# Kernel tuning notes

Hardware: AMD Instinct MI355X
Metric: run time of the kernel (lower is better)

The kernel has to match this reference:

```python
import jax, jax.numpy as jnp
import numpy as np

B, S, D = 4, 2048, 1024
HALF_PI = np.float32(np.pi / 2.0)


def setup_inputs() -> dict:
    key = jax.random.key(0)
    ks = jax.random.split(key, 12)
    std = np.float32(0.02)
    def w(k):
        return jax.random.normal(k, (D, D), dtype=jnp.float32) * std
    return {
        "x": jax.random.normal(ks[0], (B, S, D), dtype=jnp.float32),
        "W_q": w(ks[1]), "b_q": jnp.zeros((D,), jnp.float32),
        "W_k": w(ks[2]), "b_k": jnp.zeros((D,), jnp.float32),
        "W_v": w(ks[3]), "b_v": jnp.zeros((D,), jnp.float32),
        "W_t": w(ks[4]), "b_t": jnp.zeros((D,), jnp.float32),
        "W_o": w(ks[5]), "b_o": jnp.zeros((D,), jnp.float32),
        "entangle_strength": jnp.float32(0.5),
    }


def reference(x, W_q, b_q, W_k, b_k, W_v, b_v, W_t, b_t, W_o, b_o, entangle_strength):
    scale = jnp.float32(np.sqrt(D))
    Q = x @ W_q + b_q          # [B,S,D]
    K = x @ W_k + b_k
    V = x @ W_v + b_v
    # theta in [0, pi/2]; r = cos(2*theta)
    theta_q = jax.nn.sigmoid(Q @ W_t + b_t) * HALF_PI
    theta_k = jax.nn.sigmoid(K @ W_t + b_t) * HALF_PI
    r_q = jnp.cos(2.0 * theta_q)
    r_k = jnp.cos(2.0 * theta_k)
    classical = jnp.einsum("bqd,bkd->bqk", Q, K) / scale
    quantum = jnp.einsum("bqd,bkd->bqk", r_q, r_k) * entangle_strength
    attn_weights = jax.nn.softmax(classical + quantum, axis=-1)  # [B,S,S]
    # dropout: eval mode -> identity
    out = jnp.einsum("bqk,bkd->bqd", attn_weights, V)
    out = out @ W_o + b_o
    return out, attn_weights
```

## Files before the change

### kernel.cpp

```cpp
#include <hip/hip_runtime.h>
#include <cstdint>

typedef unsigned short u16;
typedef __attribute__((ext_vector_type(8))) short bf16x8;
typedef __attribute__((ext_vector_type(4))) float f32x4;

__device__ __forceinline__ u16 f2b(float x) {
  unsigned u = __float_as_uint(x);
  u += 0x7FFFu + ((u >> 16) & 1u);
  return (u16)(u >> 16);
}

__device__ __forceinline__ void gload16(const void* g, void* l) {
  __builtin_amdgcn_global_load_lds(
      (const __attribute__((address_space(1))) void*)g,
      (__attribute__((address_space(3))) void*)l, 16, 0, 0);
}

template <int N>
__device__ __forceinline__ void vmwait() {
  if constexpr (N == 0) asm volatile("s_waitcnt vmcnt(0)" ::: "memory");
  else if constexpr (N == 4) asm volatile("s_waitcnt vmcnt(4)" ::: "memory");
  else if constexpr (N == 8) asm volatile("s_waitcnt vmcnt(8)" ::: "memory");
}

__device__ __forceinline__ void stage128(const u16* __restrict__ G,
                                         long long ld, int kb,
                                         u16* Ldst, int tid) {
#pragma unroll
  for (int j = 0; j < 2; ++j) {
    const int P = j * 256 + tid;
    const int vr = P >> 3;
    const int ch = (P & 7) ^ (vr & 7);
    const int r = vr * 2 + (ch >> 2), c = ch & 3;
    gload16(G + (long long)r * ld + kb + c * 8, Ldst + P * 8);
  }
}

__device__ __forceinline__ bf16x8 fr4(const u16* R, int row, int chunk) {
  const int vr = row >> 1;
  const int ch = (((row & 1) << 2) | chunk) ^ (vr & 7);
  return *(const bf16x8*)(R + vr * 64 + ch * 8);
}

template <int EPI>
__global__ __launch_bounds__(256, 3) void e3p(
    const u16* __restrict__ A, long long lda, long long sAz,
    const u16* __restrict__ B, long long ldb, long long sBz,
    void* __restrict__ C0, void* __restrict__ C1, void* __restrict__ C2,
    long long ldc, long long sCz, int K,
    const float* __restrict__ b0, const float* __restrict__ b1,
    const float* __restrict__ b2, float preScale, const float* __restrict__ esp) {
  constexpr int HALF = 4096;
  constexpr int BUFU = 2 * HALF;
  __shared__ __align__(16) u16 lds[3 * BUFU];

  const int gx = gridDim.x, S = gx * gridDim.y;
  const int hw = blockIdx.y * gx + blockIdx.x;
  const int l = (hw & 7) * (S >> 3) + (hw >> 3);
  const int bx = l % gx, by = l / gx;
  const int z = blockIdx.z;
  const long long tM = (long long)by * 128;
  const long long tN = (long long)bx * 128;
  const u16* GA = A + z * sAz + tM * lda;
  const u16* GB = B + z * sBz + tN * ldb;
  const int tid = threadIdx.x;
  const int NT = K >> 5;

  stage128(GA, lda, 0, lds, tid);
  stage128(GB, ldb, 0, lds + HALF, tid);
  stage128(GA, lda, 32, lds + BUFU, tid);
  stage128(GB, ldb, 32, lds + BUFU + HALF, tid);

  const int wid = tid >> 6, lane = tid & 63;
  const int wr = (wid >> 1) * 64, wc = (wid & 1) * 64;
  const int lr = lane & 15, cA = lane >> 4;
  f32x4 acc[4][4] = {};

  for (int t = 0; t < NT; ++t) {
    if (t < NT - 1) vmwait<4>(); else vmwait<0>();
    __builtin_amdgcn_s_barrier();
    if (t + 2 < NT) {
      u16* nxt = lds + ((t + 2) % 3) * BUFU;
      stage128(GA, lda, (t + 2) * 32, nxt, tid);
      stage128(GB, ldb, (t + 2) * 32, nxt + HALF, tid);
    }
    const u16* cur = lds + (t % 3) * BUFU;
    bf16x8 a[4], b[4];
#pragma unroll
    for (int m = 0; m < 4; ++m) a[m] = fr4(cur, wr + m * 16 + lr, cA);
#pragma unroll
    for (int n = 0; n < 4; ++n) b[n] = fr4(cur + HALF, wc + n * 16 + lr, cA);
#pragma unroll
    for (int m = 0; m < 4; ++m)
#pragma unroll
      for (int n = 0; n < 4; ++n)
        acc[m][n] = __builtin_amdgcn_mfma_f32_16x16x32_bf16(a[m], b[n],
                                                            acc[m][n], 0, 0, 0);
  }

  const int rr = (lane >> 4) << 2;
  float ps = preScale, mul = 1.0f;
  if constexpr (EPI == 1) {
    ps = (z == 0) ? preScale : 1.0f;
    mul = (z == 0) ? esp[0] : 1.0f;
  }
#pragma unroll
  for (int m = 0; m < 4; ++m) {
#pragma unroll
    for (int n = 0; n < 4; ++n) {
      const int col = (int)tN + wc + n * 16 + lr;
#pragma unroll
      for (int r = 0; r < 4; ++r) {
        const long long row = tM + wr + m * 16 + rr + r;
        const float v = acc[m][n][r];
        if constexpr (EPI == 0) {
          const int gg = col >> 10, cc = col & 1023;
          if (gg == 0)      ((u16*)C0)[row * 2048 + cc] = f2b((v + b0[cc]) * 0.03125f);
          else if (gg == 1) ((u16*)C1)[row * 2048 + cc] = f2b(v + b1[cc]);
          else              ((u16*)C2)[row * 1024 + cc] = f2b(v + b2[cc]);
        } else if constexpr (EPI == 1) {
          const float tt = v * ps + b0[col];
          const float sg = 1.f / (1.f + __expf(-tt));
          ((u16*)C0)[z * sCz + row * ldc + col] = f2b(mul * cospif(sg));
        } else if constexpr (EPI == 2) {
          ((u16*)C0)[z * sCz + row * ldc + col] = f2b(v);
        } else if constexpr (EPI == 3) {
          ((float*)C0)[z * sCz + row * ldc + col] = v + b0[col];
        } else {
          ((float*)C0)[z * sCz + row * ldc + col] = v;
        }
      }
    }
  }
}

__global__ __launch_bounds__(256) void softmax_rows(float* __restrict__ L,
                                                    u16* __restrict__ AB) {
  const long long row = blockIdx.x;
  float4* p4 = (float4*)(L + row * 2048);
  const int tid = threadIdx.x;
  float4 a = p4[tid], b = p4[tid + 256];
  float m = fmaxf(fmaxf(fmaxf(a.x, a.y), fmaxf(a.z, a.w)),
                  fmaxf(fmaxf(b.x, b.y), fmaxf(b.z, b.w)));
#pragma unroll
  for (int o = 32; o > 0; o >>= 1) m = fmaxf(m, __shfl_xor(m, o));
  __shared__ float rmax[4], rsum[4];
  const int wid = tid >> 6, lane = tid & 63;
  if (lane == 0) rmax[wid] = m;
  __syncthreads();
  m = fmaxf(fmaxf(rmax[0], rmax[1]), fmaxf(rmax[2], rmax[3]));
  a.x = __expf(a.x - m); a.y = __expf(a.y - m);
  a.z = __expf(a.z - m); a.w = __expf(a.w - m);
  b.x = __expf(b.x - m); b.y = __expf(b.y - m);
  b.z = __expf(b.z - m); b.w = __expf(b.w - m);
  float s = a.x + a.y + a.z + a.w + b.x + b.y + b.z + b.w;
#pragma unroll
  for (int o = 32; o > 0; o >>= 1) s += __shfl_xor(s, o);
  if (lane == 0) rsum[wid] = s;
  __syncthreads();
  s = rsum[0] + rsum[1] + rsum[2] + rsum[3];
  const float inv = 1.0f / s;
  a.x *= inv; a.y *= inv; a.z *= inv; a.w *= inv;
  b.x *= inv; b.y *= inv; b.z *= inv; b.w *= inv;
  p4[tid] = a;
  p4[tid + 256] = b;
  ushort4* o4 = (ushort4*)(AB + row * 2048);
  o4[tid]       = make_ushort4(f2b(a.x), f2b(a.y), f2b(a.z), f2b(a.w));
  o4[tid + 256] = make_ushort4(f2b(b.x), f2b(b.y), f2b(b.z), f2b(b.w));
}

__global__ __launch_bounds__(256) void cvt_x(const float* __restrict__ X,
                                             u16* __restrict__ XB) {
  const int i = blockIdx.x * 256 + threadIdx.x;
  float4 v = ((const float4*)X)[i];
  ((ushort4*)XB)[i] = make_ushort4(f2b(v.x), f2b(v.y), f2b(v.z), f2b(v.w));
}

__global__ void cvt_w(const float* __restrict__ W0, const float* __restrict__ W1,
                      const float* __restrict__ W2, const float* __restrict__ W3,
                      const float* __restrict__ W4, u16* __restrict__ WT) {
  __shared__ float t[32][33];
  const int z = blockIdx.z;
  const float* W = (z == 0) ? W0 : (z == 1) ? W1 : (z == 2) ? W2 : (z == 3) ? W3 : W4;
  u16* D = WT + (long long)z * 1024 * 1024;
  const int c0 = blockIdx.x * 32, r0 = blockIdx.y * 32;
  const int tx = threadIdx.x, ty = threadIdx.y;
#pragma unroll
  for (int i = 0; i < 4; ++i)
    t[ty + i * 8][tx] = W[(long long)(r0 + ty + i * 8) * 1024 + c0 + tx];
  __syncthreads();
#pragma unroll
  for (int i = 0; i < 4; ++i)
    D[(long long)(c0 + ty + i * 8) * 1024 + r0 + tx] = f2b(t[tx][ty + i * 8]);
}

__global__ void transpose_v(const u16* __restrict__ Vb, u16* __restrict__ VT) {
  __shared__ u16 t[32][33];
  const int b = blockIdx.z;
  const u16* V = Vb + (long long)b * 2048 * 1024;
  u16* O = VT + (long long)b * 1024 * 2048;
  const int d0 = blockIdx.x * 32, s0 = blockIdx.y * 32;
  const int tx = threadIdx.x, ty = threadIdx.y;
#pragma unroll
  for (int i = 0; i < 4; ++i)
    t[ty + i * 8][tx] = V[(long long)(s0 + ty + i * 8) * 1024 + d0 + tx];
  __syncthreads();
#pragma unroll
  for (int i = 0; i < 4; ++i)
    O[(long long)(d0 + ty + i * 8) * 2048 + s0 + tx] = t[tx][ty + i * 8];
}

extern "C" void kernel_launch(void* const* d_in, const int* in_sizes, int n_in,
                              void* d_out, int out_size, void* d_ws,
                              size_t ws_size, hipStream_t stream) {
  const float* x  = (const float*)d_in[0];
  const float* Wq = (const float*)d_in[1];
  const float* bq = (const float*)d_in[2];
  const float* Wk = (const float*)d_in[3];
  const float* bk = (const float*)d_in[4];
  const float* Wv = (const float*)d_in[5];
  const float* bv = (const float*)d_in[6];
  const float* Wt = (const float*)d_in[7];
  const float* bt = (const float*)d_in[8];
  const float* Wo = (const float*)d_in[9];
  const float* bo = (const float*)d_in[10];
  const float* es = (const float*)d_in[11];

  char* ws = (char*)d_ws;
  u16* WT   = (u16*)(ws);
  u16* XB   = (u16*)(ws + 10485760);
  u16* Qcat = (u16*)(ws + 27262976);
  u16* Kcat = Qcat + 16777216;
  u16* Vb   = (u16*)(ws + 94371840);
  u16* VT   = (u16*)(ws + 111149056);
  u16* WtT  = WT + 3 * 1048576;
  u16* WoT  = WT + 4 * 1048576;
  u16* ATT  = Qcat;
  u16* AV   = XB;

  float* outO = (float*)d_out;
  float* outA = outO + 8388608;

  cvt_x<<<8192, 256, 0, stream>>>(x, XB);
  cvt_w<<<dim3(32, 32, 5), dim3(32, 8), 0, stream>>>(Wq, Wk, Wv, Wt, Wo, WT);
  e3p<0><<<dim3(24, 64, 1), 256, 0, stream>>>(
      XB, 1024, 0, WT, 1024, 0, Qcat, Kcat, Vb, 0, 0, 1024, bq, bk, bv,
      1.f, nullptr);
  e3p<1><<<dim3(8, 64, 2), 256, 0, stream>>>(
      Qcat, 2048, 16777216LL, WtT, 1024, 0, Qcat + 1024, nullptr, nullptr,
      2048, 16777216LL, 1024, bt, nullptr, nullptr, 32.f, es);
  transpose_v<<<dim3(32, 64, 4), dim3(32, 8), 0, stream>>>(Vb, VT);
  e3p<4><<<dim3(16, 16, 4), 256, 0, stream>>>(
      Qcat, 2048, 4194304LL, Kcat, 2048, 4194304LL, outA, nullptr, nullptr,
      2048, 4194304LL, 2048, nullptr, nullptr, nullptr, 1.f, nullptr);
  softmax_rows<<<8192, 256, 0, stream>>>(outA, ATT);
  e3p<2><<<dim3(8, 16, 4), 256, 0, stream>>>(
      ATT, 2048, 4194304LL, VT, 2048, 2097152LL, AV, nullptr, nullptr,
      1024, 2097152LL, 2048, nullptr, nullptr, nullptr, 1.f, nullptr);
  e3p<3><<<dim3(8, 64, 1), 256, 0, stream>>>(
      AV, 1024, 0, WoT, 1024, 0, outO, nullptr, nullptr,
      1024, 0, 1024, bo, nullptr, nullptr, 1.f, nullptr);
}
```

Measured before the change: 352.1 us.

## Fold W_t into Q/K weights, fuse theta projections into one wide GEMM, compute V transposed

Precomputes Wq·Wt and Wk·Wt (plus a folded bias) so theta_q/theta_k come straight from x in the same wide GEMM that produces Q and K. This removes the dependent second GEMM over Q/K and its reread of the Q/K buffers. V is now produced already transposed by a GEMM with swapped operands, which eliminates the separate transpose kernel. In exchange it adds small weight-product GEMMs and a bias-fold kernel, and the new wide 128x256 tile kernel uses more registers and LDS and runs at lower occupancy.

```diff
diff --git a/kernel.cpp b/kernel.cpp
--- a/kernel.cpp
+++ b/kernel.cpp
@@ -21,7 +21,7 @@
 __device__ __forceinline__ void vmwait() {
   if constexpr (N == 0) asm volatile("s_waitcnt vmcnt(0)" ::: "memory");
   else if constexpr (N == 4) asm volatile("s_waitcnt vmcnt(4)" ::: "memory");
-  else if constexpr (N == 8) asm volatile("s_waitcnt vmcnt(8)" ::: "memory");
+  else if constexpr (N == 6) asm volatile("s_waitcnt vmcnt(6)" ::: "memory");
 }
 
 __device__ __forceinline__ void stage128(const u16* __restrict__ G,
@@ -47,10 +47,8 @@
 __global__ __launch_bounds__(256, 3) void e3p(
     const u16* __restrict__ A, long long lda, long long sAz,
     const u16* __restrict__ B, long long ldb, long long sBz,
-    void* __restrict__ C0, void* __restrict__ C1, void* __restrict__ C2,
-    long long ldc, long long sCz, int K,
-    const float* __restrict__ b0, const float* __restrict__ b1,
-    const float* __restrict__ b2, float preScale, const float* __restrict__ esp) {
+    void* __restrict__ C0, long long ldc, long long sCz, int K,
+    const float* __restrict__ b0) {
   constexpr int HALF = 4096;
   constexpr int BUFU = 2 * HALF;
   __shared__ __align__(16) u16 lds[3 * BUFU];
@@ -100,11 +98,6 @@
   }
 
   const int rr = (lane >> 4) << 2;
-  float ps = preScale, mul = 1.0f;
-  if constexpr (EPI == 1) {
-    ps = (z == 0) ? preScale : 1.0f;
-    mul = (z == 0) ? esp[0] : 1.0f;
-  }
 #pragma unroll
   for (int m = 0; m < 4; ++m) {
 #pragma unroll
@@ -114,25 +107,122 @@
       for (int r = 0; r < 4; ++r) {
         const long long row = tM + wr + m * 16 + rr + r;
         const float v = acc[m][n][r];
-        if constexpr (EPI == 0) {
-          const int gg = col >> 10, cc = col & 1023;
-          if (gg == 0)      ((u16*)C0)[row * 2048 + cc] = f2b((v + b0[cc]) * 0.03125f);
-          else if (gg == 1) ((u16*)C1)[row * 2048 + cc] = f2b(v + b1[cc]);
-          else              ((u16*)C2)[row * 1024 + cc] = f2b(v + b2[cc]);
-        } else if constexpr (EPI == 1) {
-          const float tt = v * ps + b0[col];
-          const float sg = 1.f / (1.f + __expf(-tt));
-          ((u16*)C0)[z * sCz + row * ldc + col] = f2b(mul * cospif(sg));
-        } else if constexpr (EPI == 2) {
+        if constexpr (EPI == 2) {
           ((u16*)C0)[z * sCz + row * ldc + col] = f2b(v);
         } else if constexpr (EPI == 3) {
           ((float*)C0)[z * sCz + row * ldc + col] = v + b0[col];
+        } else if constexpr (EPI == 4) {
+          ((float*)C0)[z * sCz + row * ldc + col] = v;
         } else {
-          ((float*)C0)[z * sCz + row * ldc + col] = v;
+          ((u16*)C0)[z * sCz + row * ldc + col] = f2b(v + b0[row]);
         }
       }
     }
   }
+}
+
+__device__ __forceinline__ void stage_w(const u16* GA, const u16* GB,
+                                        long long lda, long long ldb,
+                                        int kb, u16* buf, int tid) {
+  stage128(GA, lda, kb, buf, tid);
+  stage128(GB, ldb, kb, buf + 4096, tid);
+  stage128(GB + 128 * ldb, ldb, kb, buf + 8192, tid);
+}
+
+__global__ __launch_bounds__(256, 2) void e3w(
+    const u16* __restrict__ A, long long lda,
+    const u16* __restrict__ B, long long ldb,
+    u16* __restrict__ Qc, u16* __restrict__ Kc, int K,
+    const float* __restrict__ b0, const float* __restrict__ b1,
+    const float* __restrict__ b2, const float* __restrict__ b3,
+    const float* __restrict__ esp) {
+  constexpr int AS = 4096, BS = 8192;
+  constexpr int BUFU = AS + BS;
+  __shared__ __align__(16) u16 lds[3 * BUFU];
+
+  const int gx = gridDim.x, S = gx * gridDim.y;
+  const int hw = blockIdx.y * gx + blockIdx.x;
+  const int l = (hw & 7) * (S >> 3) + (hw >> 3);
+  const int bx = l % gx, by = l / gx;
+  const long long tM = (long long)by * 128;
+  const long long tN = (long long)bx * 256;
+  const u16* GA = A + tM * lda;
+  const u16* GB = B + tN * ldb;
+  const int tid = threadIdx.x;
+  const int NT = K >> 5;
+
+  stage_w(GA, GB, lda, ldb, 0, lds, tid);
+  stage_w(GA, GB, lda, ldb, 32, lds + BUFU, tid);
+
+  const int wid = tid >> 6, lane = tid & 63;
+  const int wr = (wid >> 1) * 64, wc = (wid & 1) * 128;
+  const int lr = lane & 15, cA = lane >> 4;
+  f32x4 acc[4][8] = {};
+
+  for (int t = 0; t < NT; ++t) {
+    if (t < NT - 1) vmwait<6>(); else vmwait<0>();
+    __builtin_amdgcn_s_barrier();
+    if (t + 2 < NT)
+      stage_w(GA, GB, lda, ldb, (t + 2) * 32, lds + ((t + 2) % 3) * BUFU, tid);
+    const u16* cur = lds + (t % 3) * BUFU;
+    const u16* Bs = cur + AS + (wid & 1) * 4096;
+    bf16x8 a[4], b[8];
+#pragma unroll
+    for (int m = 0; m < 4; ++m) a[m] = fr4(cur, wr + m * 16 + lr, cA);
+#pragma unroll
+    for (int n = 0; n < 8; ++n) b[n] = fr4(Bs, n * 16 + lr, cA);
+#pragma unroll
+    for (int m = 0; m < 4; ++m)
+#pragma unroll
+      for (int n = 0; n < 8; ++n)
+        acc[m][n] = __builtin_amdgcn_mfma_f32_16x16x32_bf16(a[m], b[n],
+                                                            acc[m][n], 0, 0, 0);
+  }
+
+  const int rr = (lane >> 4) << 2;
+  const float es = esp[0];
+#pragma unroll
+  for (int m = 0; m < 4; ++m) {
+#pragma unroll
+    for (int n = 0; n < 8; ++n) {
+      const int col = (int)tN + wc + n * 16 + lr;
+      const int g = col >> 10, cc = col & 1023;
+#pragma unroll
+      for (int r = 0; r < 4; ++r) {
+        const long long row = tM + wr + m * 16 + rr + r;
+        const float v = acc[m][n][r];
+        if (g == 0) {
+          Qc[row * 2048 + cc] = f2b((v + b0[cc]) * 0.03125f);
+        } else if (g == 1) {
+          Kc[row * 2048 + cc] = f2b(v + b1[cc]);
+        } else if (g == 2) {
+          const float tt = v + b2[cc];
+          Qc[row * 2048 + 1024 + cc] = f2b(es * cospif(1.f / (1.f + __expf(-tt))));
+        } else {
+          const float tt = v + b3[cc];
+          Kc[row * 2048 + 1024 + cc] = f2b(cospif(1.f / (1.f + __expf(-tt))));
+        }
+      }
+    }
+  }
+}
+
+__global__ __launch_bounds__(256) void bias_fold(
+    const float* __restrict__ bq, const float* __restrict__ bk,
+    const float* __restrict__ Wt, const float* __restrict__ bt,
+    float* __restrict__ out) {
+  const int z = blockIdx.z;
+  const float* bsrc = z ? bk : bq;
+  float* dst = out + z * 1024;
+  const int il = threadIdx.x & 127, ki = threadIdx.x >> 7;
+  const int i = blockIdx.x * 128 + il;
+  float acc = 0.f;
+  for (int k = ki; k < 1024; k += 2)
+    acc += bsrc[k] * Wt[(long long)k * 1024 + i];
+  __shared__ float red[256];
+  red[threadIdx.x] = acc;
+  __syncthreads();
+  if (ki == 0) dst[i] = red[il] + red[il + 128] + bt[i];
 }
 
 __global__ __launch_bounds__(256) void softmax_rows(float* __restrict__ L,
@@ -182,10 +272,22 @@
                       const float* __restrict__ W4, u16* __restrict__ WT) {
   __shared__ float t[32][33];
   const int z = blockIdx.z;
-  const float* W = (z == 0) ? W0 : (z == 1) ? W1 : (z == 2) ? W2 : (z == 3) ? W3 : W4;
-  u16* D = WT + (long long)z * 1024 * 1024;
+  const float* W = (z == 0 || z == 5) ? W0
+                 : (z == 1 || z == 6) ? W1
+                 : (z == 2) ? W2 : (z == 3) ? W3 : W4;
+  const int slot = (z == 0) ? 0 : (z == 1) ? 1 : (z == 2) ? 4
+                 : (z == 3) ? 5 : (z == 4) ? 6 : (z == 5) ? 7 : 8;
+  u16* D = WT + ((long long)slot << 20);
   const int c0 = blockIdx.x * 32, r0 = blockIdx.y * 32;
   const int tx = threadIdx.x, ty = threadIdx.y;
+  if (z >= 5) {
+#pragma unroll
+    for (int i = 0; i < 4; ++i) {
+      const long long idx = (long long)(r0 + ty + i * 8) * 1024 + c0 + tx;
+      D[idx] = f2b(W[idx]);
+    }
+    return;
+  }
 #pragma unroll
   for (int i = 0; i < 4; ++i)
     t[ty + i * 8][tx] = W[(long long)(r0 + ty + i * 8) * 1024 + c0 + tx];
@@ -193,22 +295,6 @@
 #pragma unroll
   for (int i = 0; i < 4; ++i)
     D[(long long)(c0 + ty + i * 8) * 1024 + r0 + tx] = f2b(t[tx][ty + i * 8]);
-}
-
-__global__ void transpose_v(const u16* __restrict__ Vb, u16* __restrict__ VT) {
-  __shared__ u16 t[32][33];
-  const int b = blockIdx.z;
-  const u16* V = Vb + (long long)b * 2048 * 1024;
-  u16* O = VT + (long long)b * 1024 * 2048;
-  const int d0 = blockIdx.x * 32, s0 = blockIdx.y * 32;
-  const int tx = threadIdx.x, ty = threadIdx.y;
-#pragma unroll
-  for (int i = 0; i < 4; ++i)
-    t[ty + i * 8][tx] = V[(long long)(s0 + ty + i * 8) * 1024 + d0 + tx];
-  __syncthreads();
-#pragma unroll
-  for (int i = 0; i < 4; ++i)
-    O[(long long)(d0 + ty + i * 8) * 2048 + s0 + tx] = t[tx][ty + i * 8];
 }
 
 extern "C" void kernel_launch(void* const* d_in, const int* in_sizes, int n_in,
@@ -228,37 +314,37 @@
   const float* es = (const float*)d_in[11];
 
   char* ws = (char*)d_ws;
-  u16* WT   = (u16*)(ws);
-  u16* XB   = (u16*)(ws + 10485760);
-  u16* Qcat = (u16*)(ws + 27262976);
-  u16* Kcat = Qcat + 16777216;
-  u16* Vb   = (u16*)(ws + 94371840);
-  u16* VT   = (u16*)(ws + 111149056);
-  u16* WtT  = WT + 3 * 1048576;
-  u16* WoT  = WT + 4 * 1048576;
-  u16* ATT  = Qcat;
-  u16* AV   = XB;
+  u16* WT     = (u16*)(ws);
+  float* BQT  = (float*)(ws + 18874368);
+  u16* XB     = (u16*)(ws + 20971520);
+  u16* Qcat   = (u16*)(ws + 37748736);
+  u16* Kcat   = (u16*)(ws + 71303168);
+  u16* VT     = (u16*)(ws + 104857600);
+  u16* ATT    = Qcat;
+  u16* AV     = XB;
 
   float* outO = (float*)d_out;
   float* outA = outO + 8388608;
 
   cvt_x<<<8192, 256, 0, stream>>>(x, XB);
-  cvt_w<<<dim3(32, 32, 5), dim3(32, 8), 0, stream>>>(Wq, Wk, Wv, Wt, Wo, WT);
-  e3p<0><<<dim3(24, 64, 1), 256, 0, stream>>>(
-      XB, 1024, 0, WT, 1024, 0, Qcat, Kcat, Vb, 0, 0, 1024, bq, bk, bv,
-      1.f, nullptr);
-  e3p<1><<<dim3(8, 64, 2), 256, 0, stream>>>(
-      Qcat, 2048, 16777216LL, WtT, 1024, 0, Qcat + 1024, nullptr, nullptr,
-      2048, 16777216LL, 1024, bt, nullptr, nullptr, 32.f, es);
-  transpose_v<<<dim3(32, 64, 4), dim3(32, 8), 0, stream>>>(Vb, VT);
+  cvt_w<<<dim3(32, 32, 7), dim3(32, 8), 0, stream>>>(Wq, Wk, Wv, Wt, Wo, WT);
+  bias_fold<<<dim3(8, 1, 2), 256, 0, stream>>>(bq, bk, Wt, bt, BQT);
+  e3p<2><<<dim3(8, 8, 2), 256, 0, stream>>>(
+      WT + (5LL << 20), 1024, 0, WT + (7LL << 20), 1024, 1048576,
+      WT + (2LL << 20), 1024, 1048576, 1024, nullptr);
+  e3w<<<dim3(16, 64, 1), 256, 0, stream>>>(
+      XB, 1024, WT, 1024, Qcat, Kcat, 1024, bq, bk, BQT, BQT + 1024, es);
+  e3p<6><<<dim3(16, 8, 4), 256, 0, stream>>>(
+      WT + (4LL << 20), 1024, 0, XB, 1024, 2097152,
+      VT, 2048, 2097152, 1024, bv);
   e3p<4><<<dim3(16, 16, 4), 256, 0, stream>>>(
-      Qcat, 2048, 4194304LL, Kcat, 2048, 4194304LL, outA, nullptr, nullptr,
-      2048, 4194304LL, 2048, nullptr, nullptr, nullptr, 1.f, nullptr);
+      Qcat, 2048, 4194304, Kcat, 2048, 4194304,
+      outA, 2048, 4194304, 2048, nullptr);
   softmax_rows<<<8192, 256, 0, stream>>>(outA, ATT);
   e3p<2><<<dim3(8, 16, 4), 256, 0, stream>>>(
-      ATT, 2048, 4194304LL, VT, 2048, 2097152LL, AV, nullptr, nullptr,
-      1024, 2097152LL, 2048, nullptr, nullptr, nullptr, 1.f, nullptr);
+      ATT, 2048, 4194304, VT, 2048, 2097152,
+      AV, 1024, 2097152, 2048, nullptr);
   e3p<3><<<dim3(8, 64, 1), 256, 0, stream>>>(
-      AV, 1024, 0, WoT, 1024, 0, outO, nullptr, nullptr,
-      1024, 0, 1024, bo, nullptr, nullptr, 1.f, nullptr);
-}
+      AV, 1024, 0, WT + (6LL << 20), 1024, 0,
+      outO, 1024, 0, 1024, bo);
+}
```

Result: slower. 581.3 us (+65.1%).

## Fold W_v·W_o into one weight and drop V projection and transpose

Applied to the files above, without the earlier changes.

Uses associativity: out = A·(x·Wv + bv)·Wo + bo = A·(x·(Wv·Wo)) + (bv·Wo + bo), because softmax rows sum to one. It precomputes Wv·Wo once, computes the transposed product (WvWo)^T·x^T directly, and folds the biases into one vector. This removes the separate V projection, the V transpose and the final output projection GEMM. The QK projection is narrowed to two outputs. The cost is a small extra 1024³ weight GEMM and an extra bf16 rounding of the combined weight.

```diff
diff --git a/kernel.cpp b/kernel.cpp
--- a/kernel.cpp
+++ b/kernel.cpp
@@ -21,7 +21,6 @@
 __device__ __forceinline__ void vmwait() {
   if constexpr (N == 0) asm volatile("s_waitcnt vmcnt(0)" ::: "memory");
   else if constexpr (N == 4) asm volatile("s_waitcnt vmcnt(4)" ::: "memory");
-  else if constexpr (N == 8) asm volatile("s_waitcnt vmcnt(8)" ::: "memory");
 }
 
 __device__ __forceinline__ void stage128(const u16* __restrict__ G,
@@ -47,10 +46,10 @@
 __global__ __launch_bounds__(256, 3) void e3p(
     const u16* __restrict__ A, long long lda, long long sAz,
     const u16* __restrict__ B, long long ldb, long long sBz,
-    void* __restrict__ C0, void* __restrict__ C1, void* __restrict__ C2,
+    void* __restrict__ C0, void* __restrict__ C1,
     long long ldc, long long sCz, int K,
     const float* __restrict__ b0, const float* __restrict__ b1,
-    const float* __restrict__ b2, float preScale, const float* __restrict__ esp) {
+    float preScale, const float* __restrict__ esp) {
   constexpr int HALF = 4096;
   constexpr int BUFU = 2 * HALF;
   __shared__ __align__(16) u16 lds[3 * BUFU];
@@ -115,10 +114,9 @@
         const long long row = tM + wr + m * 16 + rr + r;
         const float v = acc[m][n][r];
         if constexpr (EPI == 0) {
-          const int gg = col >> 10, cc = col & 1023;
-          if (gg == 0)      ((u16*)C0)[row * 2048 + cc] = f2b((v + b0[cc]) * 0.03125f);
-          else if (gg == 1) ((u16*)C1)[row * 2048 + cc] = f2b(v + b1[cc]);
-          else              ((u16*)C2)[row * 1024 + cc] = f2b(v + b2[cc]);
+          const int g = col >> 10, cc = col & 1023;
+          if (g == 0) ((u16*)C0)[row * 2048 + cc] = f2b((v + b0[cc]) * 0.03125f);
+          else        ((u16*)C1)[row * 2048 + cc] = f2b(v + b1[cc]);
         } else if constexpr (EPI == 1) {
           const float tt = v * ps + b0[col];
           const float sg = 1.f / (1.f + __expf(-tt));
@@ -135,6 +133,23 @@
   }
 }
 
+__global__ __launch_bounds__(256) void bias_fold(
+    const float* __restrict__ bv, const float* __restrict__ Wo,
+    const float* __restrict__ bo, float* __restrict__ out) {
+  const int i = blockIdx.x;
+  float acc = 0.f;
+  for (int k = threadIdx.x; k < 1024; k += 256)
+    acc += bv[k] * Wo[(long long)k * 1024 + i];
+  __shared__ float red[256];
+  red[threadIdx.x] = acc;
+  __syncthreads();
+  for (int s = 128; s > 0; s >>= 1) {
+    if (threadIdx.x < s) red[threadIdx.x] += red[threadIdx.x + s];
+    __syncthreads();
+  }
+  if (threadIdx.x == 0) out[i] = red[0] + bo[i];
+}
+
 __global__ __launch_bounds__(256) void softmax_rows(float* __restrict__ L,
                                                     u16* __restrict__ AB) {
   const long long row = blockIdx.x;
@@ -177,15 +192,24 @@
   ((ushort4*)XB)[i] = make_ushort4(f2b(v.x), f2b(v.y), f2b(v.z), f2b(v.w));
 }
 
-__global__ void cvt_w(const float* __restrict__ W0, const float* __restrict__ W1,
-                      const float* __restrict__ W2, const float* __restrict__ W3,
-                      const float* __restrict__ W4, u16* __restrict__ WT) {
+__global__ void cvt_w(const float* __restrict__ Wq, const float* __restrict__ Wk,
+                      const float* __restrict__ Wt, const float* __restrict__ Wo,
+                      const float* __restrict__ Wv, u16* __restrict__ WT) {
   __shared__ float t[32][33];
   const int z = blockIdx.z;
-  const float* W = (z == 0) ? W0 : (z == 1) ? W1 : (z == 2) ? W2 : (z == 3) ? W3 : W4;
-  u16* D = WT + (long long)z * 1024 * 1024;
+  const float* W = (z == 0) ? Wq : (z == 1) ? Wk : (z == 2) ? Wt
+                 : (z == 3) ? Wo : Wv;
+  u16* D = WT + ((long long)z << 20);
   const int c0 = blockIdx.x * 32, r0 = blockIdx.y * 32;
   const int tx = threadIdx.x, ty = threadIdx.y;
+  if (z == 4) {
+#pragma unroll
+    for (int i = 0; i < 4; ++i) {
+      const long long idx = (long long)(r0 + ty + i * 8) * 1024 + c0 + tx;
+      D[idx] = f2b(W[idx]);
+    }
+    return;
+  }
 #pragma unroll
   for (int i = 0; i < 4; ++i)
     t[ty + i * 8][tx] = W[(long long)(r0 + ty + i * 8) * 1024 + c0 + tx];
@@ -193,22 +217,6 @@
 #pragma unroll
   for (int i = 0; i < 4; ++i)
     D[(long long)(c0 + ty + i * 8) * 1024 + r0 + tx] = f2b(t[tx][ty + i * 8]);
-}
-
-__global__ void transpose_v(const u16* __restrict__ Vb, u16* __restrict__ VT) {
-  __shared__ u16 t[32][33];
-  const int b = blockIdx.z;
-  const u16* V = Vb + (long long)b * 2048 * 1024;
-  u16* O = VT + (long long)b * 1024 * 2048;
-  const int d0 = blockIdx.x * 32, s0 = blockIdx.y * 32;
-  const int tx = threadIdx.x, ty = threadIdx.y;
-#pragma unroll
-  for (int i = 0; i < 4; ++i)
-    t[ty + i * 8][tx] = V[(long long)(s0 + ty + i * 8) * 1024 + d0 + tx];
-  __syncthreads();
-#pragma unroll
-  for (int i = 0; i < 4; ++i)
-    O[(long long)(d0 + ty + i * 8) * 2048 + s0 + tx] = t[tx][ty + i * 8];
 }
 
 extern "C" void kernel_launch(void* const* d_in, const int* in_sizes, int n_in,
@@ -228,37 +236,37 @@
   const float* es = (const float*)d_in[11];
 
   char* ws = (char*)d_ws;
-  u16* WT   = (u16*)(ws);
-  u16* XB   = (u16*)(ws + 10485760);
-  u16* Qcat = (u16*)(ws + 27262976);
-  u16* Kcat = Qcat + 16777216;
-  u16* Vb   = (u16*)(ws + 94371840);
-  u16* VT   = (u16*)(ws + 111149056);
-  u16* WtT  = WT + 3 * 1048576;
-  u16* WoT  = WT + 4 * 1048576;
-  u16* ATT  = Qcat;
-  u16* AV   = XB;
+  u16* WT    = (u16*)(ws);
+  float* BF  = (float*)(ws + 12582912);
+  u16* XB    = (u16*)(ws + 12587008);
+  u16* Qcat  = (u16*)(ws + 29364224);
+  u16* Kcat  = Qcat + 16777216;
+  u16* XVT   = (u16*)(ws + 96473088);
+  u16* ATT   = Qcat;
 
   float* outO = (float*)d_out;
   float* outA = outO + 8388608;
 
   cvt_x<<<8192, 256, 0, stream>>>(x, XB);
-  cvt_w<<<dim3(32, 32, 5), dim3(32, 8), 0, stream>>>(Wq, Wk, Wv, Wt, Wo, WT);
-  e3p<0><<<dim3(24, 64, 1), 256, 0, stream>>>(
-      XB, 1024, 0, WT, 1024, 0, Qcat, Kcat, Vb, 0, 0, 1024, bq, bk, bv,
-      1.f, nullptr);
+  cvt_w<<<dim3(32, 32, 5), dim3(32, 8), 0, stream>>>(Wq, Wk, Wt, Wo, Wv, WT);
+  bias_fold<<<1024, 256, 0, stream>>>(bv, Wo, bo, BF);
+  e3p<2><<<dim3(8, 8, 1), 256, 0, stream>>>(
+      WT + (3LL << 20), 1024, 0, WT + (4LL << 20), 1024, 0,
+      WT + (5LL << 20), nullptr, 1024, 0, 1024, nullptr, nullptr, 1.f, nullptr);
+  e3p<0><<<dim3(16, 64, 1), 256, 0, stream>>>(
+      XB, 1024, 0, WT, 1024, 0, Qcat, Kcat, 2048, 0, 1024,
+      bq, bk, 1.f, nullptr);
   e3p<1><<<dim3(8, 64, 2), 256, 0, stream>>>(
-      Qcat, 2048, 16777216LL, WtT, 1024, 0, Qcat + 1024, nullptr, nullptr,
-      2048, 16777216LL, 1024, bt, nullptr, nullptr, 32.f, es);
-  transpose_v<<<dim3(32, 64, 4), dim3(32, 8), 0, stream>>>(Vb, VT);
+      Qcat, 2048, 16777216, WT + (2LL << 20), 1024, 0, Qcat + 1024, nullptr,
+      2048, 16777216, 1024, bt, nullptr, 32.f, es);
+  e3p<2><<<dim3(16, 8, 4), 256, 0, stream>>>(
+      WT + (5LL << 20), 1024, 0, XB, 1024, 2097152,
+      XVT, nullptr, 2048, 2097152, 1024, nullptr, nullptr, 1.f, nullptr);
   e3p<4><<<dim3(16, 16, 4), 256, 0, stream>>>(
-      Qcat, 2048, 4194304LL, Kcat, 2048, 4194304LL, outA, nullptr, nullptr,
-      2048, 4194304LL, 2048, nullptr, nullptr, nullptr, 1.f, nullptr);
+      Qcat, 2048, 4194304, Kcat, 2048, 4194304,
+      outA, nullptr, 2048, 4194304, 2048, nullptr, nullptr, 1.f, nullptr);
   softmax_rows<<<8192, 256, 0, stream>>>(outA, ATT);
-  e3p<2><<<dim3(8, 16, 4), 256, 0, stream>>>(
-      ATT, 2048, 4194304LL, VT, 2048, 2097152LL, AV, nullptr, nullptr,
-      1024, 2097152LL, 2048, nullptr, nullptr, nullptr, 1.f, nullptr);
-  e3p<3><<<dim3(8, 64, 1), 256, 0, stream>>>(
-      AV, 1024, 0, WoT, 1024, 0, outO, nullptr, nullptr,
-      1024, 0, 1024, bo, nullptr, nullptr, 1.f, nullptr);
-}
+  e3p<3><<<dim3(8, 16, 4), 256, 0, stream>>>(
+      ATT, 2048, 4194304, XVT, 2048, 2097152,
+      outO, nullptr, 1024, 2097152, 2048, BF, nullptr, 1.f, nullptr);
+}
```

New measurement: 339.5 us. 3.6% less time.
